# Kernel optimization log

Hardware: AMD Instinct MI355X
Metric: run time of the kernel (lower is better)

Reference implementation:

```python
import jax, jax.numpy as jnp
import numpy as np

B, N, L = 1, 2048, 256
DX, DY, H = 1536, 768, 12
D = DX // H  # head_dim = 128
EPS_MOD = 1e-6   # modulated_rmsnorm eps
EPS_QK = 1e-5    # per-head RMSNorm eps


def setup_inputs() -> dict:
    key = jax.random.key(0)
    ks = jax.random.split(key, 16)
    def n(k, shape, s=1.0):
        return jax.random.normal(k, shape, dtype=jnp.float32) * s
    # rotary tables: (N, H, D//2), shared across heads
    pos = jnp.arange(N, dtype=jnp.float32)
    inv_freq = 1.0 / (10000.0 ** (jnp.arange(D // 2, dtype=jnp.float32) / (D // 2)))
    ang = pos[:, None] * inv_freq[None, :]                       # (N, D/2)
    rope_cos = jnp.broadcast_to(jnp.cos(ang)[:, None, :], (N, H, D // 2))
    rope_sin = jnp.broadcast_to(jnp.sin(ang)[:, None, :], (N, H, D // 2))
    return {
        "x": n(ks[0], (B, N, DX)),
        "y": n(ks[1], (B, L, DY)),
        "scale_x": n(ks[2], (B, DX), 0.1),
        "scale_y": n(ks[3], (B, DY), 0.1),
        "rope_cos": rope_cos,
        "rope_sin": rope_sin,
        "Wqkv_x": n(ks[4], (DX, 3 * DX), 0.02),
        "bqkv_x": jnp.zeros((3 * DX,), jnp.float32),
        "Wqkv_y": n(ks[5], (DY, 3 * DX), 0.02),
        "bqkv_y": jnp.zeros((3 * DX,), jnp.float32),
        "q_norm_x_w": jnp.ones((D,), jnp.float32),
        "k_norm_x_w": jnp.ones((D,), jnp.float32),
        "q_norm_y_w": jnp.ones((D,), jnp.float32),
        "k_norm_y_w": jnp.ones((D,), jnp.float32),
        "Wproj_x": n(ks[6], (DX, DX), 0.02),
        "bproj_x": jnp.zeros((DX,), jnp.float32),
        "Wproj_y": n(ks[7], (DX, DY), 0.02),
        "bproj_y": jnp.zeros((DY,), jnp.float32),
    }


def _rms(v, eps):
    return v * jax.lax.rsqrt(jnp.mean(v * v, axis=-1, keepdims=True) + eps)


def _rope(q, cos, sin):
    # q: (B, S, H, D); cos/sin: (S, H, D/2); even/odd interleaved rotation
    qe, qo = q[..., 0::2], q[..., 1::2]
    re = qe * cos - qo * sin
    ro = qe * sin + qo * cos
    return jnp.stack([re, ro], axis=-1).reshape(q.shape)


def reference(x, y, scale_x, scale_y, rope_cos, rope_sin,
              Wqkv_x, bqkv_x, Wqkv_y, bqkv_y,
              q_norm_x_w, k_norm_x_w, q_norm_y_w, k_norm_y_w,
              Wproj_x, bproj_x, Wproj_y, bproj_y):
    b, n, dx = x.shape
    _, l, _ = y.shape
    h, d = H, D
    # --- visual stream ---
    xm = _rms(x, EPS_MOD) * (1.0 + scale_x[:, None, :])          # modulated_rmsnorm
    qkv = (xm @ Wqkv_x + bqkv_x).reshape(b, n, 3, h, d)
    q_x, k_x, v_x = qkv[:, :, 0], qkv[:, :, 1], qkv[:, :, 2]
    q_x = _rope(_rms(q_x, EPS_QK) * q_norm_x_w, rope_cos, rope_sin)
    k_x = _rope(_rms(k_x, EPS_QK) * k_norm_x_w, rope_cos, rope_sin)
    # --- text stream ---
    ym = _rms(y, EPS_MOD) * (1.0 + scale_y[:, None, :])
    qkvy = (ym @ Wqkv_y + bqkv_y).reshape(b, l, 3, h, d)
    q_y, k_y, v_y = qkvy[:, :, 0], qkvy[:, :, 1], qkvy[:, :, 2]
    q_y = _rms(q_y, EPS_QK) * q_norm_y_w
    k_y = _rms(k_y, EPS_QK) * k_norm_y_w
    # --- joint attention over concatenated sequence (B, H, N+L, D) ---
    q = jnp.concatenate([q_x, q_y], axis=1).transpose(0, 2, 1, 3)
    k = jnp.concatenate([k_x, k_y], axis=1).transpose(0, 2, 1, 3)
    v = jnp.concatenate([v_x, v_y], axis=1).transpose(0, 2, 1, 3)
    scale = 1.0 / np.sqrt(d).astype(np.float32)
    attn = jax.nn.softmax(jnp.einsum('bhqd,bhkd->bhqk', q, k) * scale, axis=-1)
    out = jnp.einsum('bhqk,bhkd->bhqd', attn, v)
    out = out.transpose(0, 2, 1, 3).reshape(b, n + l, h * d)
    x_out = out[:, :n] @ Wproj_x + bproj_x
    y_out = out[:, n:] @ Wproj_y + bproj_y
    return (x_out, y_out)
```

## Files before the change

### kernel.cpp

```cpp
#include <hip/hip_runtime.h>

typedef unsigned short u16;
typedef __attribute__((ext_vector_type(8))) short short8;
typedef __attribute__((ext_vector_type(4))) short short4v;
typedef __attribute__((ext_vector_type(4))) float floatx4;

__device__ __forceinline__ u16 f2bf(float f) {
  return (u16)((__float_as_uint(f) + 0x8000u) >> 16);
}
__device__ __forceinline__ float bf2f(u16 v) {
  return __uint_as_float(((unsigned)v) << 16);
}
__device__ __forceinline__ unsigned cvt_pk_bf16(float a, float b) {
  unsigned r;
  asm("v_cvt_pk_bf16_f32 %0, %1, %2" : "=v"(r) : "v"(a), "v"(b));
  return r;
}

#define GLD16(g, l) __builtin_amdgcn_global_load_lds( \
    (const __attribute__((address_space(1))) void*)(g), \
    (__attribute__((address_space(3))) void*)(l), 16, 0, 0)

__global__ __launch_bounds__(256) void prep(const float* __restrict__ W0, u16* __restrict__ T0,
                                            const float* __restrict__ W1, u16* __restrict__ T1,
                                            const float* __restrict__ W2, u16* __restrict__ T2,
                                            const float* __restrict__ W3, u16* __restrict__ T3,
                                            const float* __restrict__ x, const float* __restrict__ scale_x,
                                            const float* __restrict__ y, const float* __restrict__ scale_y,
                                            u16* __restrict__ xm, u16* __restrict__ ym) {
  __shared__ float t[32][33];
  const int z = blockIdx.z;
  if (z < 4) {
    const float* in; u16* out; int K, N;
    switch (z) {
      case 0: in = W0; out = T0; K = 1536; N = 4608; break;
      case 1: in = W1; out = T1; K = 768;  N = 4608; break;
      case 2: in = W2; out = T2; K = 1536; N = 1536; break;
      default: in = W3; out = T3; K = 1536; N = 768; break;
    }
    const int n0 = blockIdx.x * 32, k0 = blockIdx.y * 32;
    if (n0 >= N || k0 >= K) return;
    const int tx = threadIdx.x, ty = threadIdx.y;
#pragma unroll
    for (int i = 0; i < 32; i += 8)
      t[ty + i][tx] = in[(size_t)(k0 + ty + i) * N + n0 + tx];
    __syncthreads();
#pragma unroll
    for (int i = 0; i < 32; i += 8)
      out[(size_t)(n0 + ty + i) * K + k0 + tx] = f2bf(t[tx][ty + i]);
  } else {
    const int row = blockIdx.y * 144 + blockIdx.x;
    if (row >= 2304) return;
    const int tid = threadIdx.y * 32 + threadIdx.x;
    const float* xr; const float* sc; u16* dst; int D;
    if (row < 2048) { D = 1536; xr = x + (size_t)row * D; sc = scale_x; dst = xm + (size_t)row * D; }
    else { D = 768; xr = y + (size_t)(row - 2048) * D; sc = scale_y; dst = ym + (size_t)(row - 2048) * D; }
    float ss = 0.f;
    for (int c = tid; c < D; c += 256) { float v = xr[c]; ss += v * v; }
    for (int off = 32; off > 0; off >>= 1) ss += __shfl_down(ss, off);
    __shared__ float red[4];
    if ((tid & 63) == 0) red[tid >> 6] = ss;
    __syncthreads();
    const float tot = red[0] + red[1] + red[2] + red[3];
    const float r = rsqrtf(tot / (float)D + 1e-6f);
    for (int c = tid; c < D; c += 256)
      dst[c] = f2bf(xr[c] * r * (1.0f + sc[c]));
  }
}

template <bool BOUT>
__global__ __launch_bounds__(256) void gemm2(const u16* __restrict__ A0, const u16* __restrict__ BT0,
                                             const float* __restrict__ bias0, void* __restrict__ C0,
                                             int M0, int N0, int K0,
                                             const u16* __restrict__ A1, const u16* __restrict__ BT1,
                                             const float* __restrict__ bias1, void* __restrict__ C1,
                                             int M1, int N1, int K1) {
  const u16 *A, *BT; const float* bias; void* Cout; int M, N, K;
  if (blockIdx.z == 0) { A = A0; BT = BT0; bias = bias0; Cout = C0; M = M0; N = N0; K = K0; }
  else { A = A1; BT = BT1; bias = bias1; Cout = C1; M = M1; N = N1; K = K1; }
  const int bm = blockIdx.y * 128, bn = blockIdx.x * 128;
  if (bm >= M || bn >= N) return;

  __shared__ __align__(16) u16 As[2][128 * 32];
  __shared__ __align__(16) u16 Bs[2][128 * 32];
  const int tid = threadIdx.x;
  const int lane = tid & 63, wave = tid >> 6;
  const int wm = (wave & 1) * 64, wn = (wave >> 1) * 64;
  const int row16 = lane & 15, quad = lane >> 4;

  floatx4 acc[4][4] = {};
  const int r0 = lane >> 2, c4 = (lane & 3) * 8;
  const u16* Ag0 = A + (size_t)(bm + wave * 16 + r0) * K + c4;
  const u16* Ag1 = A + (size_t)(bm + (wave + 4) * 16 + r0) * K + c4;
  const u16* Bg0 = BT + (size_t)(bn + wave * 16 + r0) * K + c4;
  const u16* Bg1 = BT + (size_t)(bn + (wave + 4) * 16 + r0) * K + c4;
  const int d0 = wave * 512, d1 = (wave + 4) * 512;

  GLD16(Ag0, &As[0][d0]);
  GLD16(Ag1, &As[0][d1]);
  GLD16(Bg0, &Bs[0][d0]);
  GLD16(Bg1, &Bs[0][d1]);

  int cur = 0;
  for (int k0 = 0; k0 < K; k0 += 32) {
    if (k0 + 32 < K) {
      GLD16(Ag0 + k0 + 32, &As[cur ^ 1][d0]);
      GLD16(Ag1 + k0 + 32, &As[cur ^ 1][d1]);
      GLD16(Bg0 + k0 + 32, &Bs[cur ^ 1][d0]);
      GLD16(Bg1 + k0 + 32, &Bs[cur ^ 1][d1]);
      asm volatile("s_waitcnt vmcnt(4)" ::: "memory");
    } else {
      asm volatile("s_waitcnt vmcnt(0)" ::: "memory");
    }
    __builtin_amdgcn_s_barrier();
    asm volatile("" ::: "memory");
    short8 af[4], bf[4];
#pragma unroll
    for (int i = 0; i < 4; i++) {
      af[i] = *(const short8*)&As[cur][(wm + i * 16 + row16) * 32 + quad * 8];
      bf[i] = *(const short8*)&Bs[cur][(wn + i * 16 + row16) * 32 + quad * 8];
    }
#pragma unroll
    for (int mi = 0; mi < 4; mi++)
#pragma unroll
      for (int ni = 0; ni < 4; ni++)
        acc[mi][ni] = __builtin_amdgcn_mfma_f32_16x16x32_bf16(af[mi], bf[ni], acc[mi][ni], 0, 0, 0);
    asm volatile("" ::: "memory");
    __builtin_amdgcn_s_barrier();
    cur ^= 1;
  }
#pragma unroll
  for (int mi = 0; mi < 4; mi++) {
#pragma unroll
    for (int ni = 0; ni < 4; ni++) {
      const int col = bn + wn + ni * 16 + row16;
      const float b = bias[col];
      const int row0 = bm + wm + mi * 16 + quad * 4;
#pragma unroll
      for (int r = 0; r < 4; r++) {
        const float v = acc[mi][ni][r] + b;
        if constexpr (BOUT)
          ((u16*)Cout)[(size_t)(row0 + r) * N + col] = f2bf(v);
        else
          ((float*)Cout)[(size_t)(row0 + r) * N + col] = v;
      }
    }
  }
}

__global__ __launch_bounds__(256) void qkv_post(const u16* __restrict__ qkvx,
                                                const u16* __restrict__ qkvy,
                                                const float* __restrict__ qnwx, const float* __restrict__ knwx,
                                                const float* __restrict__ qnwy, const float* __restrict__ knwy,
                                                const float* __restrict__ rcos, const float* __restrict__ rsin,
                                                u16* __restrict__ Q, u16* __restrict__ Kb, u16* __restrict__ Vt) {
  const int s0 = blockIdx.x * 32, h = blockIdx.y;
  const int tid = threadIdx.x, wave = tid >> 6, lane = tid & 63;
  const int sl = wave * 8 + (lane >> 3);
  const int s = s0 + sl;
  const int d0 = (lane & 7) * 16;
  const bool isx = s < 2048;
  const u16* base = isx ? (qkvx + (size_t)s * 4608) : (qkvy + (size_t)(s - 2048) * 4608);

  const short8 qv0 = *(const short8*)(base + h * 128 + d0);
  const short8 qv1 = *(const short8*)(base + h * 128 + d0 + 8);
  const short8 kv0 = *(const short8*)(base + 1536 + h * 128 + d0);
  const short8 kv1 = *(const short8*)(base + 1536 + h * 128 + d0 + 8);
  const short8 vv0 = *(const short8*)(base + 3072 + h * 128 + d0);
  const short8 vv1 = *(const short8*)(base + 3072 + h * 128 + d0 + 8);

  float q[16], k[16];
#pragma unroll
  for (int j = 0; j < 8; j++) {
    q[j] = bf2f((u16)qv0[j]); q[j + 8] = bf2f((u16)qv1[j]);
    k[j] = bf2f((u16)kv0[j]); k[j + 8] = bf2f((u16)kv1[j]);
  }
  float sq = 0.f, sk = 0.f;
#pragma unroll
  for (int j = 0; j < 16; j++) { sq += q[j] * q[j]; sk += k[j] * k[j]; }
#pragma unroll
  for (int off = 1; off <= 4; off <<= 1) { sq += __shfl_xor(sq, off); sk += __shfl_xor(sk, off); }
  const float rq = rsqrtf(sq * (1.f / 128.f) + 1e-5f);
  const float rk = rsqrtf(sk * (1.f / 128.f) + 1e-5f);

  const float* qw = isx ? qnwx : qnwy;
  const float* kw = isx ? knwx : knwy;
#pragma unroll
  for (int j = 0; j < 16; j++) {
    q[j] = q[j] * rq * qw[d0 + j];
    k[j] = k[j] * rk * kw[d0 + j];
  }
  if (isx) {
    const float* cb = rcos + ((size_t)s * 12 + h) * 64 + (d0 >> 1);
    const float* sb = rsin + ((size_t)s * 12 + h) * 64 + (d0 >> 1);
#pragma unroll
    for (int p = 0; p < 8; p++) {
      const float c = cb[p], sn = sb[p];
      const float qe = q[2 * p], qo = q[2 * p + 1];
      const float ke = k[2 * p], ko = k[2 * p + 1];
      q[2 * p] = qe * c - qo * sn; q[2 * p + 1] = qe * sn + qo * c;
      k[2 * p] = ke * c - ko * sn; k[2 * p + 1] = ke * sn + ko * c;
    }
  }
  u16 qo16[16], ko16[16];
#pragma unroll
  for (int j = 0; j < 16; j++) {
    qo16[j] = f2bf(q[j] * 0.12751737942f);
    ko16[j] = f2bf(k[j]);
  }
  const size_t o = ((size_t)h * 2304 + s) * 128 + d0;
  *(short8*)(Q + o) = *(const short8*)&qo16[0];
  *(short8*)(Q + o + 8) = *(const short8*)&qo16[8];
  *(short8*)(Kb + o) = *(const short8*)&ko16[0];
  *(short8*)(Kb + o + 8) = *(const short8*)&ko16[8];

  __shared__ u16 vlds[128][33];
#pragma unroll
  for (int j = 0; j < 8; j++) {
    vlds[d0 + j][sl] = (u16)vv0[j];
    vlds[d0 + 8 + j][sl] = (u16)vv1[j];
  }
  __syncthreads();
  const int row = tid >> 1, sc = (tid & 1) * 16;
  u16 tmp[16];
#pragma unroll
  for (int j = 0; j < 16; j++) tmp[j] = vlds[row][sc + j];
  u16* vdst = Vt + ((size_t)h * 128 + row) * 2304 + s0 + sc;
  *(short8*)vdst = *(const short8*)&tmp[0];
  *(short8*)(vdst + 8) = *(const short8*)&tmp[8];
}

__global__ __launch_bounds__(256, 3) void attn(const u16* __restrict__ Q, const u16* __restrict__ Kb,
                                               const u16* __restrict__ Vt,
                                               u16* __restrict__ Opart,
                                               float* __restrict__ Mp, float* __restrict__ Lp) {
  const int bid = blockIdx.x;
  const int xcd = bid & 7, local = bid >> 3;
  const int slot = local / 18, qt = local % 18;
  const int combo = slot * 8 + xcd;
  if (combo >= 36) return;
  const int h = combo % 12, split = combo / 12;
  const int q0 = qt * 128;
  const int tid = threadIdx.x, lane = tid & 63, wave = tid >> 6;
  const int row16 = lane & 15, quad = lane >> 4;
  const u16* Qh = Q + (size_t)h * 2304 * 128;
  const u16* Kh = Kb + (size_t)h * 2304 * 128;
  const u16* Vh = Vt + (size_t)h * 128 * 2304;

  __shared__ __align__(16) u16 Ks[64 * 128];
  __shared__ __align__(16) u16 Vs[128 * 64];
  __shared__ __align__(16) u16 Ps[4][32 * 64];

  short8 qf[2][4];
#pragma unroll
  for (int g = 0; g < 2; g++) {
    const u16* qrow = Qh + (size_t)(q0 + wave * 32 + g * 16 + row16) * 128;
#pragma unroll
    for (int kk = 0; kk < 4; kk++) qf[g][kk] = *(const short8*)(qrow + kk * 32 + quad * 8);
  }
  floatx4 oacc[2][8] = {};
  float m_i[2] = {-1e30f, -1e30f}, l_i[2] = {0.f, 0.f};

  const u16* Kp[4]; const u16* Vp[4];
#pragma unroll
  for (int i = 0; i < 4; i++) {
    const int j = i * 4 + wave;
    const int krow = j * 4 + (lane >> 4);
    const int kcol = ((lane & 15) ^ (krow & 7)) * 8;
    const int vrow = j * 8 + (lane >> 3);
    const int vcol = ((lane & 7) ^ (vrow & 7)) * 8;
    Kp[i] = Kh + (size_t)krow * 128 + kcol;
    Vp[i] = Vh + (size_t)vrow * 2304 + vcol;
  }
  const int sw = row16 & 7;
  const int kbeg = split * 768, kend = kbeg + 768;

  for (int kt = kbeg; kt < kend; kt += 64) {
    __syncthreads();
#pragma unroll
    for (int i = 0; i < 4; i++) {
      GLD16(Kp[i] + (size_t)kt * 128, Ks + (i * 4 + wave) * 512);
      GLD16(Vp[i] + kt, Vs + (i * 4 + wave) * 512);
    }
    __syncthreads();

    floatx4 sacc[2][4] = {};
#pragma unroll
    for (int mk = 0; mk < 4; mk++) {
#pragma unroll
      for (int kk = 0; kk < 4; kk++) {
        const int c = (4 * kk + quad) ^ sw;
        const short8 kfrag = *(const short8*)&Ks[(mk * 16 + row16) * 128 + c * 8];
        sacc[0][mk] = __builtin_amdgcn_mfma_f32_16x16x32_bf16(kfrag, qf[0][kk], sacc[0][mk], 0, 0, 0);
        sacc[1][mk] = __builtin_amdgcn_mfma_f32_16x16x32_bf16(kfrag, qf[1][kk], sacc[1][mk], 0, 0, 0);
      }
    }
#pragma unroll
    for (int g = 0; g < 2; g++) {
      float mx = sacc[g][0][0];
#pragma unroll
      for (int mk = 0; mk < 4; mk++)
#pragma unroll
        for (int r = 0; r < 4; r++) mx = fmaxf(mx, sacc[g][mk][r]);
      mx = fmaxf(mx, __shfl_xor(mx, 16));
      mx = fmaxf(mx, __shfl_xor(mx, 32));
      if (__any(mx > m_i[g] + 8.f)) {
        const float mnew = fmaxf(m_i[g], mx);
        const float alpha = __builtin_amdgcn_exp2f(m_i[g] - mnew);
        m_i[g] = mnew;
        const float a0 = __shfl(alpha, quad * 4 + 0);
        const float a1 = __shfl(alpha, quad * 4 + 1);
        const float a2 = __shfl(alpha, quad * 4 + 2);
        const float a3 = __shfl(alpha, quad * 4 + 3);
#pragma unroll
        for (int nd = 0; nd < 8; nd++) {
          oacc[g][nd][0] *= a0; oacc[g][nd][1] *= a1; oacc[g][nd][2] *= a2; oacc[g][nd][3] *= a3;
        }
        l_i[g] *= alpha;
      }
      float s = 0.f;
#pragma unroll
      for (int mk = 0; mk < 4; mk++)
#pragma unroll
        for (int r = 0; r < 4; r++) {
          const float p = __builtin_amdgcn_exp2f(sacc[g][mk][r] - m_i[g]);
          sacc[g][mk][r] = p;
          s += p;
        }
      s += __shfl_xor(s, 16);
      s += __shfl_xor(s, 32);
      l_i[g] += s;
    }

#pragma unroll
    for (int g = 0; g < 2; g++)
#pragma unroll
      for (int mk = 0; mk < 4; mk++) {
        const int subp = (4 * mk + quad) ^ (sw << 1);
        uint2 pk;
        pk.x = cvt_pk_bf16(sacc[g][mk][0], sacc[g][mk][1]);
        pk.y = cvt_pk_bf16(sacc[g][mk][2], sacc[g][mk][3]);
        *(uint2*)&Ps[wave][(g * 16 + row16) * 64 + subp * 4] = pk;
      }
    const int pc0 = quad ^ sw, pc1 = (4 + quad) ^ sw;
    short8 pf[2][2];
#pragma unroll
    for (int g = 0; g < 2; g++) {
      pf[g][0] = *(const short8*)&Ps[wave][(g * 16 + row16) * 64 + pc0 * 8];
      pf[g][1] = *(const short8*)&Ps[wave][(g * 16 + row16) * 64 + pc1 * 8];
    }
#pragma unroll
    for (int nd = 0; nd < 8; nd++) {
      const short8 vf0 = *(const short8*)&Vs[(nd * 16 + row16) * 64 + pc0 * 8];
      const short8 vf1 = *(const short8*)&Vs[(nd * 16 + row16) * 64 + pc1 * 8];
      oacc[0][nd] = __builtin_amdgcn_mfma_f32_16x16x32_bf16(pf[0][0], vf0, oacc[0][nd], 0, 0, 0);
      oacc[0][nd] = __builtin_amdgcn_mfma_f32_16x16x32_bf16(pf[0][1], vf1, oacc[0][nd], 0, 0, 0);
      oacc[1][nd] = __builtin_amdgcn_mfma_f32_16x16x32_bf16(pf[1][0], vf0, oacc[1][nd], 0, 0, 0);
      oacc[1][nd] = __builtin_amdgcn_mfma_f32_16x16x32_bf16(pf[1][1], vf1, oacc[1][nd], 0, 0, 0);
    }
  }
#pragma unroll
  for (int g = 0; g < 2; g++) {
    const size_t base = (size_t)(split * 12 + h) * 2304 + q0 + wave * 32 + g * 16;
#pragma unroll
    for (int nd = 0; nd < 8; nd++)
#pragma unroll
      for (int r = 0; r < 4; r++)
        Opart[(base + quad * 4 + r) * 128 + nd * 16 + row16] = f2bf(oacc[g][nd][r]);
    if (lane < 16) { Mp[base + lane] = m_i[g]; Lp[base + lane] = l_i[g]; }
  }
}

__global__ __launch_bounds__(256) void attn_combine(const u16* __restrict__ Opart,
                                                    const float* __restrict__ Mp,
                                                    const float* __restrict__ Lp,
                                                    u16* __restrict__ attnout) {
  const int idx = blockIdx.x * 256 + threadIdx.x;
  const int dd = (idx & 31) * 4;
  const int hq = idx >> 5;
  const int h = hq % 12, q = hq / 12;
  size_t b[3]; float ms[3], ls[3];
  float m = -1e30f;
#pragma unroll
  for (int s = 0; s < 3; s++) {
    b[s] = (size_t)(s * 12 + h) * 2304 + q;
    ms[s] = Mp[b[s]]; ls[s] = Lp[b[s]];
    m = fmaxf(m, ms[s]);
  }
  float w[3], denom = 0.f;
#pragma unroll
  for (int s = 0; s < 3; s++) { w[s] = exp2f(ms[s] - m); denom += ls[s] * w[s]; }
  const float inv = 1.0f / denom;
  float ox = 0.f, oy = 0.f, oz = 0.f, ow = 0.f;
#pragma unroll
  for (int s = 0; s < 3; s++) {
    const short4v o = *(const short4v*)&Opart[b[s] * 128 + dd];
    ox += bf2f((u16)o[0]) * w[s]; oy += bf2f((u16)o[1]) * w[s];
    oz += bf2f((u16)o[2]) * w[s]; ow += bf2f((u16)o[3]) * w[s];
  }
  short4v out;
  out[0] = (short)f2bf(ox * inv);
  out[1] = (short)f2bf(oy * inv);
  out[2] = (short)f2bf(oz * inv);
  out[3] = (short)f2bf(ow * inv);
  *(short4v*)&attnout[(size_t)idx * 4] = out;
}

extern "C" void kernel_launch(void* const* d_in, const int* in_sizes, int n_in,
                              void* d_out, int out_size, void* d_ws, size_t ws_size,
                              hipStream_t stream) {
  const float* x        = (const float*)d_in[0];
  const float* y        = (const float*)d_in[1];
  const float* scale_x  = (const float*)d_in[2];
  const float* scale_y  = (const float*)d_in[3];
  const float* rope_cos = (const float*)d_in[4];
  const float* rope_sin = (const float*)d_in[5];
  const float* Wqkv_x   = (const float*)d_in[6];
  const float* bqkv_x   = (const float*)d_in[7];
  const float* Wqkv_y   = (const float*)d_in[8];
  const float* bqkv_y   = (const float*)d_in[9];
  const float* qnwx     = (const float*)d_in[10];
  const float* knwx     = (const float*)d_in[11];
  const float* qnwy     = (const float*)d_in[12];
  const float* knwy     = (const float*)d_in[13];
  const float* Wproj_x  = (const float*)d_in[14];
  const float* bproj_x  = (const float*)d_in[15];
  const float* Wproj_y  = (const float*)d_in[16];
  const float* bproj_y  = (const float*)d_in[17];
  float* out = (float*)d_out;

  char* ws = (char*)d_ws;
  size_t off = 0;
  auto take = [&](size_t bytes) { char* p = ws + off; off += (bytes + 255) & ~(size_t)255; return p; };
  u16* WqkvxT  = (u16*)take((size_t)4608 * 1536 * 2);
  u16* WqkvyT  = (u16*)take((size_t)4608 * 768 * 2);
  u16* WprojxT = (u16*)take((size_t)1536 * 1536 * 2);
  u16* WprojyT = (u16*)take((size_t)768 * 1536 * 2);
  u16* xm      = (u16*)take((size_t)2048 * 1536 * 2);
  u16* ym      = (u16*)take((size_t)256 * 768 * 2);
  u16* qkvx    = (u16*)take((size_t)2048 * 4608 * 2);
  u16* qkvy    = (u16*)take((size_t)256 * 4608 * 2);
  u16* Qb      = (u16*)take((size_t)12 * 2304 * 128 * 2);
  u16* Kb      = (u16*)take((size_t)12 * 2304 * 128 * 2);
  u16* Vt      = (u16*)take((size_t)12 * 128 * 2304 * 2);
  u16* attnout = (u16*)take((size_t)2304 * 1536 * 2);
  u16* Opart   = (u16*)take((size_t)3 * 12 * 2304 * 128 * 2);
  float* Mp    = (float*)take((size_t)3 * 12 * 2304 * 4);
  float* Lp    = (float*)take((size_t)3 * 12 * 2304 * 4);

  prep<<<dim3(144, 48, 5), dim3(32, 8), 0, stream>>>(Wqkv_x, WqkvxT, Wqkv_y, WqkvyT,
                                                     Wproj_x, WprojxT, Wproj_y, WprojyT,
                                                     x, scale_x, y, scale_y, xm, ym);

  gemm2<true><<<dim3(36, 16, 2), 256, 0, stream>>>(xm, WqkvxT, bqkv_x, qkvx, 2048, 4608, 1536,
                                                   ym, WqkvyT, bqkv_y, qkvy, 256, 4608, 768);

  qkv_post<<<dim3(72, 12), 256, 0, stream>>>(qkvx, qkvy, qnwx, knwx, qnwy, knwy,
                                             rope_cos, rope_sin, Qb, Kb, Vt);

  attn<<<dim3(720), 256, 0, stream>>>(Qb, Kb, Vt, Opart, Mp, Lp);
  attn_combine<<<(2304 * 1536 / 4) / 256, 256, 0, stream>>>(Opart, Mp, Lp, attnout);

  gemm2<false><<<dim3(12, 16, 2), 256, 0, stream>>>(attnout, WprojxT, bproj_x, out, 2048, 1536, 1536,
                                                    attnout + (size_t)2048 * 1536, WprojyT, bproj_y,
                                                    out + (size_t)2048 * 1536, 256, 768, 1536);
  (void)in_sizes; (void)n_in; (void)out_size; (void)ws_size;
}
```

Baseline: 299.6 us.

## Triple-buffer GEMM loads and read V fragments directly from global in attention

The GEMM moves from double to triple buffering in LDS, prefetching two K-steps ahead with a matching waitcnt, so global latency is better hidden. The attention kernel no longer stages V tiles in shared memory. Each wave loads its V fragments straight from global (transposed V) into registers. This cuts LDS traffic and footprint, but every wave re-reads V from global/L2 instead of sharing one staged copy. The uncoalesced 16-byte row-strided loads may also add latency.

```diff
diff --git a/kernel.cpp b/kernel.cpp
--- a/kernel.cpp
+++ b/kernel.cpp
@@ -81,8 +81,8 @@
   const int bm = blockIdx.y * 128, bn = blockIdx.x * 128;
   if (bm >= M || bn >= N) return;
 
-  __shared__ __align__(16) u16 As[2][128 * 32];
-  __shared__ __align__(16) u16 Bs[2][128 * 32];
+  __shared__ __align__(16) u16 As[3][128 * 32];
+  __shared__ __align__(16) u16 Bs[3][128 * 32];
   const int tid = threadIdx.x;
   const int lane = tid & 63, wave = tid >> 6;
   const int wm = (wave & 1) * 64, wn = (wave >> 1) * 64;
@@ -100,14 +100,21 @@
   GLD16(Ag1, &As[0][d1]);
   GLD16(Bg0, &Bs[0][d0]);
   GLD16(Bg1, &Bs[0][d1]);
+  GLD16(Ag0 + 32, &As[1][d0]);
+  GLD16(Ag1 + 32, &As[1][d1]);
+  GLD16(Bg0 + 32, &Bs[1][d0]);
+  GLD16(Bg1 + 32, &Bs[1][d1]);
 
   int cur = 0;
   for (int k0 = 0; k0 < K; k0 += 32) {
-    if (k0 + 32 < K) {
-      GLD16(Ag0 + k0 + 32, &As[cur ^ 1][d0]);
-      GLD16(Ag1 + k0 + 32, &As[cur ^ 1][d1]);
-      GLD16(Bg0 + k0 + 32, &Bs[cur ^ 1][d0]);
-      GLD16(Bg1 + k0 + 32, &Bs[cur ^ 1][d1]);
+    if (k0 + 64 < K) {
+      int nxt2 = cur + 2; if (nxt2 >= 3) nxt2 -= 3;
+      GLD16(Ag0 + k0 + 64, &As[nxt2][d0]);
+      GLD16(Ag1 + k0 + 64, &As[nxt2][d1]);
+      GLD16(Bg0 + k0 + 64, &Bs[nxt2][d0]);
+      GLD16(Bg1 + k0 + 64, &Bs[nxt2][d1]);
+      asm volatile("s_waitcnt vmcnt(8)" ::: "memory");
+    } else if (k0 + 32 < K) {
       asm volatile("s_waitcnt vmcnt(4)" ::: "memory");
     } else {
       asm volatile("s_waitcnt vmcnt(0)" ::: "memory");
@@ -127,7 +134,7 @@
         acc[mi][ni] = __builtin_amdgcn_mfma_f32_16x16x32_bf16(af[mi], bf[ni], acc[mi][ni], 0, 0, 0);
     asm volatile("" ::: "memory");
     __builtin_amdgcn_s_barrier();
-    cur ^= 1;
+    cur += 1; if (cur >= 3) cur -= 3;
   }
 #pragma unroll
   for (int mi = 0; mi < 4; mi++) {
@@ -248,7 +255,6 @@
   const u16* Vh = Vt + (size_t)h * 128 * 2304;
 
   __shared__ __align__(16) u16 Ks[64 * 128];
-  __shared__ __align__(16) u16 Vs[128 * 64];
   __shared__ __align__(16) u16 Ps[4][32 * 64];
 
   short8 qf[2][4];
@@ -261,27 +267,23 @@
   floatx4 oacc[2][8] = {};
   float m_i[2] = {-1e30f, -1e30f}, l_i[2] = {0.f, 0.f};
 
-  const u16* Kp[4]; const u16* Vp[4];
+  const u16* Kp[4];
 #pragma unroll
   for (int i = 0; i < 4; i++) {
     const int j = i * 4 + wave;
     const int krow = j * 4 + (lane >> 4);
     const int kcol = ((lane & 15) ^ (krow & 7)) * 8;
-    const int vrow = j * 8 + (lane >> 3);
-    const int vcol = ((lane & 7) ^ (vrow & 7)) * 8;
     Kp[i] = Kh + (size_t)krow * 128 + kcol;
-    Vp[i] = Vh + (size_t)vrow * 2304 + vcol;
-  }
+  }
+  const u16* vb = Vh + (size_t)row16 * 2304 + quad * 8;
   const int sw = row16 & 7;
   const int kbeg = split * 768, kend = kbeg + 768;
 
   for (int kt = kbeg; kt < kend; kt += 64) {
     __syncthreads();
 #pragma unroll
-    for (int i = 0; i < 4; i++) {
+    for (int i = 0; i < 4; i++)
       GLD16(Kp[i] + (size_t)kt * 128, Ks + (i * 4 + wave) * 512);
-      GLD16(Vp[i] + kt, Vs + (i * 4 + wave) * 512);
-    }
     __syncthreads();
 
     floatx4 sacc[2][4] = {};
@@ -349,10 +351,11 @@
       pf[g][0] = *(const short8*)&Ps[wave][(g * 16 + row16) * 64 + pc0 * 8];
       pf[g][1] = *(const short8*)&Ps[wave][(g * 16 + row16) * 64 + pc1 * 8];
     }
+    const u16* vkt = vb + kt;
 #pragma unroll
     for (int nd = 0; nd < 8; nd++) {
-      const short8 vf0 = *(const short8*)&Vs[(nd * 16 + row16) * 64 + pc0 * 8];
-      const short8 vf1 = *(const short8*)&Vs[(nd * 16 + row16) * 64 + pc1 * 8];
+      const short8 vf0 = *(const short8*)(vkt + (size_t)(nd * 16) * 2304);
+      const short8 vf1 = *(const short8*)(vkt + (size_t)(nd * 16) * 2304 + 32);
       oacc[0][nd] = __builtin_amdgcn_mfma_f32_16x16x32_bf16(pf[0][0], vf0, oacc[0][nd], 0, 0, 0);
       oacc[0][nd] = __builtin_amdgcn_mfma_f32_16x16x32_bf16(pf[0][1], vf1, oacc[0][nd], 0, 0, 0);
       oacc[1][nd] = __builtin_amdgcn_mfma_f32_16x16x32_bf16(pf[1][0], vf0, oacc[1][nd], 0, 0, 0);
```

New measurement: 329.6 us. +10.0%, slower.
